# Optimization experiments

Measured on AMD Instinct MI355X. Metric: run time of the kernel, lower is better.

Reference implementation:

```python
import jax, jax.numpy as jnp
import numpy as np

B, S, E, H, F = 4, 1024, 1024, 16, 4096
D = E // H
DEPTH = 3
EPS_LN = 1e-5
EPS_ENT = 1e-6


def setup_inputs() -> dict:
    key = jax.random.key(0)
    ks = jax.random.split(key, 32)
    def w(k, shp, s=0.02):
        return (jax.random.normal(k, shp) * s).astype(jnp.float32)
    z = lambda *shp: jnp.zeros(shp, jnp.float32)
    inp = {
        'x': jax.random.normal(ks[0], (B, S, E), jnp.float32),
        # self-referential attention
        'sr_w': w(ks[1], (E, E)), 'sr_b': z(E),
        'q_w': w(ks[2], (E, E)), 'q_b': z(E),
        'k_w': w(ks[3], (E, E)), 'k_b': z(E),
        'v_w': w(ks[4], (E, E)), 'v_b': z(E),
        'o_w': w(ks[5], (E, E)), 'o_b': z(E),
        'ref_gate': jnp.float32(0.5),
        # quantum-classical interface
        'c_w': w(ks[6], (E, E)), 'c_b': z(E),
        'qp_w': w(ks[7], (E, E)), 'qp_b': z(E),
        'ig_w': w(ks[8], (2 * E, E)), 'ig_b': z(E),
        'temperature': jnp.float32(1.0),
        # entropy regulator
        'kp_w': w(ks[9], (E, E)), 'kp_b': z(E),
        'ee_w': w(ks[10], (E, 1)), 'ee_b': z(1),
        'eta': jnp.float32(0.1),
        # ffn
        'f1_w': w(ks[11], (E, F)), 'f1_b': z(F),
        'f2_w': w(ks[12], (F, E)), 'f2_b': z(E),
        # layernorms
        'ln1_g': jnp.ones(E, jnp.float32), 'ln1_b': z(E),
        'ln2_g': jnp.ones(E, jnp.float32), 'ln2_b': z(E),
        'ln3_g': jnp.ones(E, jnp.float32), 'ln3_b': z(E),
        # observer
        'obs_w': w(ks[13], (E, E)), 'obs_b': z(E),
        'obs_gate': jnp.float32(0.2),
    }
    return inp


def _lin(x, W, b):
    return x @ W + b


def _ln(x, g, b):
    m = jnp.mean(x, -1, keepdims=True)
    v = jnp.var(x, -1, keepdims=True)
    return (x - m) * jax.lax.rsqrt(v + EPS_LN) * g + b


def _layer(x, p):
    ks = jax.lax.stop_gradient(x)  # knowledge_state = x.detach()
    scale = 1.0 / (D ** 0.5)
    for _ in range(DEPTH):  # fixed small recursion depth
        # --- self-referential attention on norm1(x) ---
        xn = _ln(x, p['ln1_g'], p['ln1_b'])
        xr = xn + p['ref_gate'] * _lin(xn, p['sr_w'], p['sr_b'])
        b, s, _ = xn.shape
        q = _lin(xr, p['q_w'], p['q_b']).reshape(b, s, H, D)
        k = _lin(xr, p['k_w'], p['k_b']).reshape(b, s, H, D)
        v = _lin(xn, p['v_w'], p['v_b']).reshape(b, s, H, D)
        scores = jnp.einsum('bqhd,bkhd->bhqk', q, k) * scale  # [B,H,S,S]
        aw = jax.nn.softmax(scores, axis=-1)
        ao = jnp.einsum('bhqk,bkhd->bqhd', aw, v).reshape(b, s, E)
        quantum = _lin(ao, p['o_w'], p['o_b'])
        # --- FFN on norm2(x) (dropout = identity, eval mode) ---
        xn2 = _ln(x, p['ln2_g'], p['ln2_b'])
        h = jax.nn.gelu(_lin(xn2, p['f1_w'], p['f1_b']), approximate=False)
        classical = _lin(h, p['f2_w'], p['f2_b'])
        # --- quantum-classical interface ---
        c_proj = _lin(classical, p['c_w'], p['c_b'])
        q_proj = _lin(quantum, p['qp_w'], p['qp_b'])
        gate = jax.nn.sigmoid(_lin(jnp.concatenate([c_proj, q_proj], -1), p['ig_w'], p['ig_b']))
        sim = jnp.einsum('bqe,bke->bqk', c_proj, q_proj) / (E ** 0.5)  # [B,S,S]
        attw = jax.nn.softmax(sim / p['temperature'], axis=-1)
        transfer = jnp.einsum('bqk,bke->bqe', attw, quantum)
        iface = classical + gate * transfer
        # --- entropy regulator ---
        logp = jax.nn.log_softmax(iface, axis=-1)
        entropy = -jnp.sum(jnp.exp(logp) * logp, -1, keepdims=True)
        neg_entropy = _lin(ks, p['kp_w'], p['kp_b'])
        bal = jax.nn.sigmoid(_lin(iface, p['ee_w'], p['ee_b']))
        regulated = iface + p['eta'] * bal * (neg_entropy / (entropy + EPS_ENT))
        # --- residual + observer feedback + knowledge update ---
        x = x + regulated
        x = x + p['obs_gate'] * _lin(x, p['obs_w'], p['obs_b'])
        ks = ks + 0.1 * (x - ks)
    x = _ln(x, p['ln3_g'], p['ln3_b'])
    return x, ks


def reference(x, sr_w, sr_b, q_w, q_b, k_w, k_b, v_w, v_b, o_w, o_b, ref_gate,
              c_w, c_b, qp_w, qp_b, ig_w, ig_b, temperature,
              kp_w, kp_b, ee_w, ee_b, eta,
              f1_w, f1_b, f2_w, f2_b,
              ln1_g, ln1_b, ln2_g, ln2_b, ln3_g, ln3_b,
              obs_w, obs_b, obs_gate):
    p = dict(sr_w=sr_w, sr_b=sr_b, q_w=q_w, q_b=q_b, k_w=k_w, k_b=k_b,
             v_w=v_w, v_b=v_b, o_w=o_w, o_b=o_b, ref_gate=ref_gate,
             c_w=c_w, c_b=c_b, qp_w=qp_w, qp_b=qp_b, ig_w=ig_w, ig_b=ig_b,
             temperature=temperature, kp_w=kp_w, kp_b=kp_b, ee_w=ee_w, ee_b=ee_b,
             eta=eta, f1_w=f1_w, f1_b=f1_b, f2_w=f2_w, f2_b=f2_b,
             ln1_g=ln1_g, ln1_b=ln1_b, ln2_g=ln2_g, ln2_b=ln2_b,
             ln3_g=ln3_g, ln3_b=ln3_b, obs_w=obs_w, obs_b=obs_b, obs_gate=obs_gate)
    return _layer(x, p)
```

## Files before the change

kernel.cpp:

```cpp
#include <hip/hip_runtime.h>
#include <hip/hip_bf16.h>
#include <cmath>


typedef unsigned short u16;
typedef short v8s __attribute__((ext_vector_type(8)));
typedef float v4f __attribute__((ext_vector_type(4)));
typedef unsigned short u16x4 __attribute__((ext_vector_type(4)));

#define DEV __device__ __forceinline__

DEV float b2f(u16 u) { return __uint_as_float(((unsigned int)u) << 16); }
DEV u16 f2b(float f) {
    unsigned int x = __float_as_uint(f);
    return (u16)((x + 0x7fffu + ((x >> 16) & 1u)) >> 16);
}
DEV bool badf(float f) { return ((__float_as_uint(f) >> 23) & 0xFF) == 0xFF; }

DEV void async16(const void* g, void* l) {
    __builtin_amdgcn_global_load_lds((const __attribute__((address_space(1))) void*)g,
                                     (__attribute__((address_space(3))) void*)l, 16, 0, 0);
}

struct InArr { const void* p[37]; int n[37]; };
struct BJobs { int si[20]; int off[20]; int n[20]; };
struct GJ2 { const u16* jA; const u16* jB; const u16* jbias; u16* jout; };

#define CLS_CAP 131072

__global__ void reset_k(int* diag, int* cnt) {
    if (threadIdx.x == 0) *diag = 0x7FFFFFFF;
    if (threadIdx.x < 80) cnt[threadIdx.x] = 0;
}

__global__ void classify_k(InArr A, int* cnt) {
    int i = blockIdx.y;
    int n = A.n[i];
    if (n <= 1) return;
    const u16* q = (const u16*)A.p[i];
    long pairs = n >> 1;
    int wild = 0, pz = 0;
    if (pairs > (long)CLS_CAP) {
        long chunk = CLS_CAP / gridDim.x;
        long p0 = (long)blockIdx.x * (pairs / gridDim.x);
        for (long j = p0 + threadIdx.x; j < p0 + chunk; j += blockDim.x) {
            u16 w0 = q[2 * j], w1 = q[2 * j + 1];
            wild += ((w0 & 0x7FFF) >= 0x5000) + ((w1 & 0x7FFF) >= 0x5000);
            pz += (w0 == 0 && w1 >= 0x3000 && w1 <= 0x4100) ? 1 : 0;
        }
    } else {
        long stride = (long)gridDim.x * blockDim.x;
        for (long j = (long)blockIdx.x * blockDim.x + threadIdx.x; j < pairs; j += stride) {
            u16 w0 = q[2 * j], w1 = q[2 * j + 1];
            wild += ((w0 & 0x7FFF) >= 0x5000) + ((w1 & 0x7FFF) >= 0x5000);
            pz += (w0 == 0 && w1 >= 0x3000 && w1 <= 0x4100) ? 1 : 0;
        }
    }
#pragma unroll
    for (int off = 1; off < 64; off <<= 1) {
        wild += __shfl_xor(wild, off);
        pz += __shfl_xor(pz, off);
    }
    if ((threadIdx.x & 63) == 0) {
        atomicAdd(&cnt[2 * i], wild);
        atomicAdd(&cnt[2 * i + 1], pz);
    }
}

__global__ void finalize_k(InArr A, const int* cnt, int* flags) {
    int i = threadIdx.x;
    if (i < 37) {
        int n = A.n[i];
        int f = 0;
        if (n > 1) {
            long pairs = (long)n >> 1;
            long wthr, pthr;
            if (pairs > (long)CLS_CAP) { wthr = (2L * CLS_CAP) >> 6; pthr = (long)CLS_CAP >> 2; }
            else { wthr = (long)n >> 6; pthr = (long)n >> 3; }
            f = (cnt[2 * i] > wthr) || (cnt[2 * i + 1] > pthr);
        }
        flags[i] = f;
    }
}

DEV float dec_scalar(const u16* p) {
    float bf = b2f(p[0]);
    if (bf > 0.0009765625f && bf < 8.0f) return bf;
    unsigned int w = (((unsigned int)p[1]) << 16) | (unsigned int)p[0];
    return __uint_as_float(w);
}

__global__ void decode_scalars_k(const u16* rg, const u16* tp, const u16* et,
                                 const u16* og, float* out)
{
    if (threadIdx.x == 0 && blockIdx.x == 0) {
        out[0] = dec_scalar(rg);
        out[1] = dec_scalar(tp);
        out[2] = dec_scalar(et);
        out[3] = dec_scalar(og);
    }
}

__global__ void cvt1d_k(InArr A, BJobs J, const int* flags, u16* BIA) {
    int j = blockIdx.y;
    int n = J.n[j];
    int si = J.si[j];
    const void* src = A.p[si];
    u16* dst = BIA + (long)J.off[j] * 1024;
    int f = flags[si];
    int stride = gridDim.x * blockDim.x;
    for (int i = blockIdx.x * blockDim.x + threadIdx.x; i < n; i += stride) {
        dst[i] = f ? f2b(((const float*)src)[i]) : ((const u16*)src)[i];
    }
}

__global__ void chk_scal_k(const float* scal, int* diag) {
    if (threadIdx.x == 0) {
        for (int i = 0; i < 4; i++) {
            float v = scal[i];
            if (!(v > 0.f && v < 8.f)) atomicMin(diag, 3);
        }
    }
}

__global__ void fin32_k(float* out, long n4, const int* diag) {
    long stride = (long)gridDim.x * blockDim.x;
    long i0 = (long)blockIdx.x * blockDim.x + threadIdx.x;
    v4f* o4 = (v4f*)out;
    for (long i = i0; i < n4; i += stride) {
        v4f v = o4[i];
        bool b = false;
#pragma unroll
        for (int j = 0; j < 4; j++) b |= badf(v[j]);
        if (b) {
#pragma unroll
            for (int j = 0; j < 4; j++) if (badf(v[j])) v[j] = 0.f;
            o4[i] = v;
        }
    }
    if (i0 == 0) {
        int d = *diag;
        if (d != 0x7FFFFFFF) out[0] = 200.f + 4.f * (float)(d < 70 ? d : 70);
    }
}

__global__ void small_k(float* out, int code) {
    if (threadIdx.x == 0 && blockIdx.x == 0) out[0] = 900.f + 4.f * code;
}

__global__ __launch_bounds__(256) void f2c_k(const float* __restrict__ a, const float* __restrict__ b,
                                             const u16* __restrict__ bias, u16* __restrict__ out,
                                             int stage, int* __restrict__ diag)
{
    long i0 = ((long)blockIdx.x * 256 + threadIdx.x) * 4;
    v4f va = *(const v4f*)(a + i0);
    v4f vb = *(const v4f*)(b + i0);
    int colb = (int)(i0 & 1023);
    bool bad = false;
    u16x4 o;
#pragma unroll
    for (int j = 0; j < 4; j++) {
        float r = va[j] + vb[j] + b2f(bias[colb + j]);
        bad |= badf(r);
        o[j] = f2b(r);
    }
    *(u16x4*)(out + i0) = o;
    if (__ballot(bad) && (threadIdx.x & 63) == 0) atomicMin(diag, stage);
}

template <int EPI>
__global__ __launch_bounds__(512) void gemm_bt(
    const u16* __restrict__ A, int lda, long sA,
    const u16* __restrict__ A2, int ksplit,
    const u16* __restrict__ Bt, int ldb, long sB,
    const u16* __restrict__ bias,
    u16* __restrict__ obf, float* __restrict__ of32, int ldc, long sC,
    int K,
    const float* __restrict__ scp,
    const u16* __restrict__ aux,
    float* __restrict__ xaux, float* __restrict__ ksf, u16* __restrict__ ksb,
    float* __restrict__ kso,
    GJ2 J2,
    int stage, int* __restrict__ diag)
{
    __shared__ __align__(16) u16 As[128 * 32];
    __shared__ __align__(16) u16 Bs[128 * 32];
    const int tid = threadIdx.x;
    const int w = tid >> 6, l = tid & 63;
    const int lr = l & 15, lq = l >> 4;

    const int gx = gridDim.x, gy = gridDim.y;
    const int nwg = gx * gy * (int)gridDim.z;
    int flat = blockIdx.x + gx * (blockIdx.y + gy * blockIdx.z);
    int qq = nwg >> 3, rr = nwg & 7;
    int xcd = flat & 7, loc = flat >> 3;
    int nf = (xcd < rr ? xcd * (qq + 1) : rr * (qq + 1) + (xcd - rr) * qq) + loc;
    const int bx = nf % gx;
    int tmp = nf / gx;
    const int by = tmp % gy;
    int z = tmp / gy;

    const u16* Aj = A; const u16* Bj = Bt; const u16* biasj = bias; u16* obfj = obf;
    if (J2.jA) {
        if (z == 1) { Aj = J2.jA; Bj = J2.jB; biasj = J2.jbias; obfj = J2.jout; }
        z = 0;
    }

    const int m0 = by * 128, n0 = bx * 128;
    const u16* Az = Aj + (long)z * sA;
    const u16* Bz = Bj + (long)z * sB;
    const int wm = (w >> 2) * 64, wn = (w & 3) * 32;

    v4f zero4 = {0.f, 0.f, 0.f, 0.f};
    v4f acc[4][2];
#pragma unroll
    for (int i = 0; i < 4; i++)
#pragma unroll
        for (int j = 0; j < 2; j++) acc[i][j] = zero4;

    const int srow = tid >> 2, scc = (tid & 3) * 8;
    for (int k0 = 0; k0 < K; k0 += 32) {
        __syncthreads();
        const u16* Ab = (k0 < ksplit) ? (Az + k0) : (A2 + (k0 - ksplit));
        async16(Ab + (long)(m0 + srow) * lda + scc, (char*)As + w * 1024);
        async16(Bz + (long)(n0 + srow) * ldb + k0 + scc, (char*)Bs + w * 1024);
        __syncthreads();
        v8s av[4], bv[2];
#pragma unroll
        for (int mi = 0; mi < 4; mi++) av[mi] = *(const v8s*)(As + (wm + mi * 16 + lr) * 32 + lq * 8);
#pragma unroll
        for (int ni = 0; ni < 2; ni++) bv[ni] = *(const v8s*)(Bs + (wn + ni * 16 + lr) * 32 + lq * 8);
#pragma unroll
        for (int mi = 0; mi < 4; mi++)
#pragma unroll
            for (int ni = 0; ni < 2; ni++)
                acc[mi][ni] = __builtin_amdgcn_mfma_f32_16x16x32_bf16(av[mi], bv[ni], acc[mi][ni], 0, 0, 0);
    }

    float gsv = 0.f;
    if (EPI == 4 || EPI == 5 || EPI == 6) gsv = scp[0];
    if (EPI == 4) gsv = fmaxf(gsv, 1e-8f);
    bool bad = false;
#pragma unroll
    for (int mi = 0; mi < 4; mi++) {
        int row = m0 + wm + mi * 16 + lq * 4;
#pragma unroll
        for (int ni = 0; ni < 2; ni++) {
            int col = n0 + wn + ni * 16 + lr;
            float bb = biasj ? b2f(biasj[col]) : 0.f;
#pragma unroll
            for (int r = 0; r < 4; r++) {
                float v = acc[mi][ni][r] + bb;
                if (EPI == 6 || EPI == 7) {
                    long rbase = (long)(row + r) * 1024;
                    float res;
                    if (col < 1024) {
                        res = (EPI == 6) ? (b2f(aux[rbase + col]) + gsv * v) : v;
                        bad |= badf(res);
                        obfj[rbase + col] = f2b(res);
                    } else {
                        res = v;
                        bad |= badf(res);
                        J2.jout[rbase + col - 1024] = f2b(res);
                    }
                } else {
                    long idx = (long)z * sC + (long)(row + r) * ldc + col;
                    float res = v;
                    if (EPI == 2) res = 0.5f * v * (1.f + erff(v * 0.70710678118654752f));
                    else if (EPI == 3) res = 1.f / (1.f + expf(-v));
                    else if (EPI == 4) res = v * (0.03125f / gsv);
                    else if (EPI == 5) {
                        float xv = xaux[idx];
                        float nx = xv + gsv * v;
                        xaux[idx] = nx;
                        float kv = ksf[idx];
                        float kn = kv + 0.1f * (nx - kv);
                        ksf[idx] = kn;
                        ksb[idx] = f2b(kn);
                        if (kso) kso[idx] = kn;
                        bad |= badf(kn);
                        res = nx;
                    }
                    bad |= badf(res);
                    if (obfj) obfj[idx] = f2b(res);
                    if (of32) of32[idx] = res;
                }
            }
        }
    }
    if (__ballot(bad) && l == 0) atomicMin(diag, stage);
}

__global__ __launch_bounds__(256) void flash_k(
    const u16* __restrict__ q, const u16* __restrict__ k, const u16* __restrict__ v,
    u16* __restrict__ ao, int stage, int* __restrict__ diag)
{
    __shared__ __align__(16) u16 Ks[64 * 64];
    __shared__ __align__(16) u16 Vt[64 * 64];
    __shared__ __align__(16) u16 Pw[4 * 16 * 64];
    const int tid = threadIdx.x, w = tid >> 6, l = tid & 63;
    const int lr = l & 15, lq = l >> 4;
    const int bh = blockIdx.y, b = bh >> 4, h = bh & 15;
    const long rowbase = (long)b * 1024;
    const int h64 = h * 64;
    const int q0 = blockIdx.x * 64;

    const u16* Qp = q + (rowbase + q0 + w * 16 + lr) * 1024 + h64;
    v8s aq0 = *(const v8s*)(Qp + lq * 8);
    v8s aq1 = *(const v8s*)(Qp + 32 + lq * 8);

    v4f zero4 = {0.f, 0.f, 0.f, 0.f};
    v4f oacc[4];
    float m_r[4], l_r[4];
#pragma unroll
    for (int i = 0; i < 4; i++) { oacc[i] = zero4; m_r[i] = -INFINITY; l_r[i] = 0.f; }

    const int ss = lr & 7;
    const int colk = (lq ^ ss) << 3;
    u16* Pp = Pw + w * (16 * 64);

    for (int kt = 0; kt < 16; kt++) {
        __syncthreads();
        const long kbase = rowbase + kt * 64;
#pragma unroll
        for (int p = 0; p < 2; p++) {
            int c = p * 256 + tid;
            int row = c >> 3;
            int sl = (c & 7) ^ (row & 7);
            async16(k + (kbase + row) * 1024 + h64 + sl * 8, (char*)Ks + p * 4096 + w * 1024);
            int cc = (c & 7) * 8;
            v8s vv = *(const v8s*)(v + (kbase + row) * 1024 + h64 + cc);
#pragma unroll
            for (int j = 0; j < 8; j++) {
                int d = cc + j;
                int g = (d & 7) ^ ((d >> 3) & 7);
                Vt[((d << 6) + row) ^ (g << 3)] = (u16)vv[j];
            }
        }
        __syncthreads();

        v4f s[4];
#pragma unroll
        for (int nt = 0; nt < 4; nt++) {
            const u16* Kr = Ks + ((nt * 16 + lr) << 6);
            v8s b0 = *(const v8s*)(Kr + colk);
            v8s b1 = *(const v8s*)(Kr + (colk ^ 32));
            v4f t = zero4;
            t = __builtin_amdgcn_mfma_f32_16x16x32_bf16(aq0, b0, t, 0, 0, 0);
            t = __builtin_amdgcn_mfma_f32_16x16x32_bf16(aq1, b1, t, 0, 0, 0);
            s[nt] = t;
        }
#pragma unroll
        for (int r = 0; r < 4; r++) {
#pragma unroll
            for (int nt = 0; nt < 4; nt++) s[nt][r] *= 0.125f;
            float mx = fmaxf(fmaxf(s[0][r], s[1][r]), fmaxf(s[2][r], s[3][r]));
#pragma unroll
            for (int off = 1; off < 16; off <<= 1) mx = fmaxf(mx, __shfl_xor(mx, off));
            float mn = fmaxf(m_r[r], mx);
            float al = __expf(m_r[r] - mn);
            float rs = 0.f;
            int qrow = lq * 4 + r;
            int pbase = qrow << 6;
            int pswz = (qrow & 7) << 3;
#pragma unroll
            for (int nt = 0; nt < 4; nt++) {
                float pv = __expf(s[nt][r] - mn);
                rs += pv;
                Pp[pbase + ((nt * 16 + lr) ^ pswz)] = f2b(pv);
            }
#pragma unroll
            for (int off = 1; off < 16; off <<= 1) rs += __shfl_xor(rs, off);
            l_r[r] = l_r[r] * al + rs;
            m_r[r] = mn;
#pragma unroll
            for (int nt = 0; nt < 4; nt++) oacc[nt][r] *= al;
        }
        const u16* Pr = Pp + (lr << 6);
        v8s pa0 = *(const v8s*)(Pr + colk);
        v8s pa1 = *(const v8s*)(Pr + (colk ^ 32));
#pragma unroll
        for (int nt = 0; nt < 4; nt++) {
            const u16* Vr = Vt + ((nt * 16 + lr) << 6);
            int gv = (ss ^ (2 * nt + (lr >> 3))) << 3;
            int colv = (lq << 3) ^ gv;
            v8s vb0 = *(const v8s*)(Vr + colv);
            v8s vb1 = *(const v8s*)(Vr + (colv ^ 32));
            oacc[nt] = __builtin_amdgcn_mfma_f32_16x16x32_bf16(pa0, vb0, oacc[nt], 0, 0, 0);
            oacc[nt] = __builtin_amdgcn_mfma_f32_16x16x32_bf16(pa1, vb1, oacc[nt], 0, 0, 0);
        }
    }
    bool bad = false;
#pragma unroll
    for (int r = 0; r < 4; r++) {
        float inv = 1.f / l_r[r];
#pragma unroll
        for (int nt = 0; nt < 4; nt++) {
            float val = oacc[nt][r] * inv;
            bad |= badf(val);
            ao[(rowbase + q0 + w * 16 + lq * 4 + r) * 1024 + h64 + nt * 16 + lr] = f2b(val);
        }
    }
    if (__ballot(bad) && l == 0) atomicMin(diag, stage);
}

template <int F32OUT>
__global__ __launch_bounds__(256) void ln_k(const float* __restrict__ x,
                                            const u16* __restrict__ g, const u16* __restrict__ bt,
                                            u16* __restrict__ outb, float* __restrict__ outf,
                                            int stage, int* __restrict__ diag)
{
    __shared__ float red[8];
    int row = blockIdx.x, t = threadIdx.x, w = t >> 6;
    const float* xr = x + (long)row * 1024;
    float v[4], s = 0.f, sq = 0.f;
#pragma unroll
    for (int i = 0; i < 4; i++) { v[i] = xr[i * 256 + t]; s += v[i]; sq += v[i] * v[i]; }
#pragma unroll
    for (int off = 1; off < 64; off <<= 1) { s += __shfl_xor(s, off); sq += __shfl_xor(sq, off); }
    if ((t & 63) == 0) { red[w] = s; red[4 + w] = sq; }
    __syncthreads();
    float S = red[0] + red[1] + red[2] + red[3];
    float SQ = red[4] + red[5] + red[6] + red[7];
    float mean = S * (1.f / 1024.f);
    float var = fmaxf(SQ * (1.f / 1024.f) - mean * mean, 0.f);
    float rs = rsqrtf(var + 1e-5f);
    bool bad = false;
#pragma unroll
    for (int i = 0; i < 4; i++) {
        int e = i * 256 + t;
        float r = (v[i] - mean) * rs * b2f(g[e]) + b2f(bt[e]);
        bad |= badf(r);
        if (F32OUT) outf[(long)row * 1024 + e] = r;
        else outb[(long)row * 1024 + e] = f2b(r);
    }
    if (__ballot(bad) && (t & 63) == 0) atomicMin(diag, stage);
}

__global__ __launch_bounds__(256) void rowfuse_k(
    const u16* __restrict__ cls, const u16* __restrict__ gate, const float* __restrict__ tr,
    const u16* __restrict__ ne, const u16* __restrict__ eew, const u16* __restrict__ eeb,
    const float* __restrict__ eta_p, float* __restrict__ xbuf, u16* __restrict__ x1b,
    int stage, int* __restrict__ diag)
{
    __shared__ float red[16];
    int row = blockIdx.x, t = threadIdx.x, w = t >> 6;
    long base = (long)row * 1024;
    float ifc[4];
#pragma unroll
    for (int i = 0; i < 4; i++) {
        int e = i * 256 + t;
        ifc[i] = b2f(cls[base + e]) + b2f(gate[base + e]) * tr[base + e];
    }
    float mx = fmaxf(fmaxf(ifc[0], ifc[1]), fmaxf(ifc[2], ifc[3]));
#pragma unroll
    for (int off = 1; off < 64; off <<= 1) mx = fmaxf(mx, __shfl_xor(mx, off));
    if ((t & 63) == 0) red[w] = mx;
    __syncthreads();
    float MX = fmaxf(fmaxf(red[0], red[1]), fmaxf(red[2], red[3]));
    float s1 = 0.f, s2 = 0.f, dot = 0.f;
#pragma unroll
    for (int i = 0; i < 4; i++) {
        int e = i * 256 + t;
        float ex = expf(ifc[i] - MX);
        s1 += ex; s2 += ex * ifc[i]; dot += ifc[i] * b2f(eew[e]);
    }
#pragma unroll
    for (int off = 1; off < 64; off <<= 1) {
        s1 += __shfl_xor(s1, off); s2 += __shfl_xor(s2, off); dot += __shfl_xor(dot, off);
    }
    if ((t & 63) == 0) { red[4 + w] = s1; red[8 + w] = s2; red[12 + w] = dot; }
    __syncthreads();
    float S1 = red[4] + red[5] + red[6] + red[7];
    float S2 = red[8] + red[9] + red[10] + red[11];
    float DT = red[12] + red[13] + red[14] + red[15];
    float logZ = MX + logf(S1);
    float ent = logZ - S2 / S1;
    float bal = 1.f / (1.f + expf(-(DT + b2f(eeb[0]))));
    float fac = eta_p[0] * bal / (ent + 1e-6f);
    bool bad = false;
#pragma unroll
    for (int i = 0; i < 4; i++) {
        int e = i * 256 + t;
        float rg = ifc[i] + fac * b2f(ne[base + e]);
        float x1 = xbuf[base + e] + rg;
        bad |= badf(x1);
        xbuf[base + e] = x1;
        x1b[base + e] = f2b(x1);
    }
    if (__ballot(bad) && (t & 63) == 0) atomicMin(diag, stage);
}

__global__ __launch_bounds__(256) void softmax_k(const float* __restrict__ sim, u16* __restrict__ out,
                                                 int stage, int* __restrict__ diag)
{
    __shared__ float red[8];
    int row = blockIdx.x, t = threadIdx.x, w = t >> 6;
    long base = (long)row * 1024;
    float v[4];
#pragma unroll
    for (int i = 0; i < 4; i++) v[i] = sim[base + i * 256 + t];
    float mx = fmaxf(fmaxf(v[0], v[1]), fmaxf(v[2], v[3]));
#pragma unroll
    for (int off = 1; off < 64; off <<= 1) mx = fmaxf(mx, __shfl_xor(mx, off));
    if ((t & 63) == 0) red[w] = mx;
    __syncthreads();
    float MX = fmaxf(fmaxf(red[0], red[1]), fmaxf(red[2], red[3]));
    float s = 0.f;
#pragma unroll
    for (int i = 0; i < 4; i++) { v[i] = expf(v[i] - MX); s += v[i]; }
#pragma unroll
    for (int off = 1; off < 64; off <<= 1) s += __shfl_xor(s, off);
    if ((t & 63) == 0) red[4 + w] = s;
    __syncthreads();
    float inv = 1.f / (red[4] + red[5] + red[6] + red[7]);
    bool bad = false;
#pragma unroll
    for (int i = 0; i < 4; i++) {
        float o = v[i] * inv;
        bad |= badf(o);
        out[base + i * 256 + t] = f2b(o);
    }
    if (__ballot(bad) && (t & 63) == 0) atomicMin(diag, stage);
}

__global__ void transpose_ft_k(const void* __restrict__ in, u16* __restrict__ out,
                               int R, int C, const int* __restrict__ flags, int idx,
                               int* __restrict__ diag)
{
    __shared__ u16 tile[32][33];
    int f = flags[idx];
    int x = blockIdx.x * 32 + threadIdx.x;
    int y0 = blockIdx.y * 32;
#pragma unroll
    for (int j = 0; j < 4; j++) {
        long src = (long)(y0 + threadIdx.y + j * 8) * C + x;
        tile[threadIdx.y + j * 8][threadIdx.x] =
            f ? f2b(((const float*)in)[src]) : ((const u16*)in)[src];
    }
    __syncthreads();
    int ox = y0 + threadIdx.x;
    int oy0 = blockIdx.x * 32;
    bool bad = false;
#pragma unroll
    for (int j = 0; j < 4; j++) {
        u16 u = tile[threadIdx.x][threadIdx.y + j * 8];
        bad |= ((u & 0x7FFF) >= 0x7F80);
        out[(long)(oy0 + threadIdx.y + j * 8) * R + ox] = u;
    }
    if (__ballot(bad) && ((threadIdx.y * 32 + threadIdx.x) & 63) == 0) atomicMin(diag, 2);
}

__global__ void transpose_k(const u16* __restrict__ in, u16* __restrict__ out,
                            int R, int C, long sIn, long sOut)
{
    __shared__ u16 tile[32][33];
    int z = blockIdx.z;
    in += (long)z * sIn; out += (long)z * sOut;
    int x = blockIdx.x * 32 + threadIdx.x;
    int y0 = blockIdx.y * 32;
#pragma unroll
    for (int j = 0; j < 4; j++)
        tile[threadIdx.y + j * 8][threadIdx.x] = in[(long)(y0 + threadIdx.y + j * 8) * C + x];
    __syncthreads();
    int ox = y0 + threadIdx.x;
    int oy0 = blockIdx.x * 32;
#pragma unroll
    for (int j = 0; j < 4; j++)
        out[(long)(oy0 + threadIdx.y + j * 8) * R + ox] = tile[threadIdx.x][threadIdx.y + j * 8];
}

__global__ __launch_bounds__(256) void init_k(const void* __restrict__ xin, const int* __restrict__ flags,
                                              float* __restrict__ xbuf,
                                              float* __restrict__ ksf, u16* __restrict__ ksb,
                                              int* __restrict__ diag)
{
    int t = threadIdx.x;
    int f = flags[0];
    long base = (long)blockIdx.x * 1024;
    bool bad = false;
#pragma unroll
    for (int i = 0; i < 4; i++) {
        long idx = base + i * 256 + t;
        float xv = f ? ((const float*)xin)[idx] : b2f(((const u16*)xin)[idx]);
        bad |= badf(xv);
        xbuf[idx] = xv; ksf[idx] = xv; ksb[idx] = f2b(xv);
    }
    if (__ballot(bad) && (t & 63) == 0) atomicMin(diag, 1);
}

extern "C" void kernel_launch(void* const* d_in, const int* in_sizes, int n_in,
                              void* d_out, int out_size, void* d_ws, size_t ws_size,
                              hipStream_t stream)
{
    const size_t MB = 1u << 20;
    float* outf = (float*)d_out;
    if (ws_size < 192 * MB) {
        int code = (int)(ws_size >> 25); if (code > 9) code = 9;
        small_k<<<1, 64, 0, stream>>>(outf, code);
        return;
    }
    const u16* s_refg = (const u16*)d_in[11];
    const u16* s_temp = (const u16*)d_in[18];
    const u16* s_eta  = (const u16*)d_in[23];
    const u16* s_obsg = (const u16*)d_in[36];

    InArr IA;
    for (int i = 0; i < 37; i++) { IA.p[i] = d_in[i]; IA.n[i] = (i < n_in) ? in_sizes[i] : 0; }

    char* ws = (char*)d_ws;
    u16* srT  = (u16*)(ws + 0 * MB);
    u16* vT   = (u16*)(ws + 2 * MB);
    u16* qT   = (u16*)(ws + 4 * MB);
    u16* kT   = (u16*)(ws + 6 * MB);
    u16* oT   = (u16*)(ws + 8 * MB);
    u16* cT   = (u16*)(ws + 10 * MB);
    u16* qpT  = (u16*)(ws + 12 * MB);
    u16* kpT  = (u16*)(ws + 14 * MB);
    u16* obsT = (u16*)(ws + 16 * MB);
    u16* igT  = (u16*)(ws + 18 * MB);
    u16* f1T  = (u16*)(ws + 22 * MB);
    u16* f2T  = (u16*)(ws + 30 * MB);
    float* scal = (float*)(ws + 38 * MB);
    int* diag  = (int*)(ws + 38 * MB + 64);
    int* flags = (int*)(ws + 38 * MB + 128);
    int* cnt   = (int*)(ws + 38 * MB + 512);
    u16* BIA   = (u16*)(ws + 38 * MB + 8192);
    u16* c_bsr = BIA + 0*1024,  *c_bv = BIA + 1*1024;
    u16* c_bq  = BIA + 2*1024,  *c_bk = BIA + 3*1024;
    u16* c_bo  = BIA + 4*1024,  *c_bc = BIA + 5*1024;
    u16* c_bqp = BIA + 6*1024,  *c_big = BIA + 7*1024, *c_bkp = BIA + 8*1024;
    u16* c_bobs= BIA + 9*1024,  *c_bf2 = BIA + 10*1024;
    u16* c_g1  = BIA + 11*1024, *c_be1 = BIA + 12*1024;
    u16* c_g2  = BIA + 13*1024, *c_be2 = BIA + 14*1024;
    u16* c_g3  = BIA + 15*1024, *c_be3 = BIA + 16*1024;
    u16* c_eew = BIA + 17*1024, *c_eeb = BIA + 18*1024;
    u16* c_bf1 = BIA + 19*1024;
    float* xbuf = (float*)(ws + 40 * MB);
    float* ksf  = (float*)(ws + 56 * MB);
    u16* ksb    = (u16*)(ws + 72 * MB);
    u16* xn     = (u16*)(ws + 80 * MB);
    u16* xn2    = (u16*)(ws + 88 * MB);
    u16* xr     = (u16*)(ws + 96 * MB);
    u16* qb     = (u16*)(ws + 104 * MB);
    u16* kb     = (u16*)(ws + 112 * MB);
    u16* vb     = (u16*)(ws + 120 * MB);
    u16* aob    = (u16*)(ws + 128 * MB);
    u16* quant  = (u16*)(ws + 136 * MB);
    u16* hb     = (u16*)(ws + 144 * MB);
    float* simf = (float*)(ws + 144 * MB);
    float* trf  = (float*)(ws + 160 * MB);
    u16* clsb   = (u16*)(ws + 176 * MB);
    u16* neb    = (u16*)(ws + 184 * MB);
    float* f2pa = (float*)(ws + 104 * MB);
    float* f2pb = (float*)(ws + 120 * MB);
    u16* quantT = xn;
    u16* cpb = qb;  u16* qpb = kb;  u16* gateb = vb;  u16* attw = aob;  u16* x1b = xr;

    const long BS1 = 1024L * 1024L;
    const int KBIG = 1 << 30;
    dim3 tb(32, 8), blk(256), gblk(512);
    GJ2 J0 = {nullptr, nullptr, nullptr, nullptr};

    auto G = [&](int epi, int gx, int gy, int gz,
                 const u16* A, int lda, long sA, const u16* A2, int ksp,
                 const u16* Bt, int ldb, long sB, const u16* bias,
                 u16* obf, float* of32, int ldc, long sC, int K,
                 const float* scp, const u16* aux, float* xa, float* kf, u16* kb2, float* kso,
                 GJ2 J2, int stg) {
        dim3 grid(gx, gy, gz);
        switch (epi) {
            case 0: gemm_bt<0><<<grid, gblk, 0, stream>>>(A, lda, sA, A2, ksp, Bt, ldb, sB, bias, obf, of32, ldc, sC, K, scp, aux, xa, kf, kb2, kso, J2, stg, diag); break;
            case 2: gemm_bt<2><<<grid, gblk, 0, stream>>>(A, lda, sA, A2, ksp, Bt, ldb, sB, bias, obf, of32, ldc, sC, K, scp, aux, xa, kf, kb2, kso, J2, stg, diag); break;
            case 3: gemm_bt<3><<<grid, gblk, 0, stream>>>(A, lda, sA, A2, ksp, Bt, ldb, sB, bias, obf, of32, ldc, sC, K, scp, aux, xa, kf, kb2, kso, J2, stg, diag); break;
            case 4: gemm_bt<4><<<grid, gblk, 0, stream>>>(A, lda, sA, A2, ksp, Bt, ldb, sB, bias, obf, of32, ldc, sC, K, scp, aux, xa, kf, kb2, kso, J2, stg, diag); break;
            case 5: gemm_bt<5><<<grid, gblk, 0, stream>>>(A, lda, sA, A2, ksp, Bt, ldb, sB, bias, obf, of32, ldc, sC, K, scp, aux, xa, kf, kb2, kso, J2, stg, diag); break;
            case 6: gemm_bt<6><<<grid, gblk, 0, stream>>>(A, lda, sA, A2, ksp, Bt, ldb, sB, bias, obf, of32, ldc, sC, K, scp, aux, xa, kf, kb2, kso, J2, stg, diag); break;
            case 7: gemm_bt<7><<<grid, gblk, 0, stream>>>(A, lda, sA, A2, ksp, Bt, ldb, sB, bias, obf, of32, ldc, sC, K, scp, aux, xa, kf, kb2, kso, J2, stg, diag); break;
            case 8: gemm_bt<8><<<grid, gblk, 0, stream>>>(A, lda, sA, A2, ksp, Bt, ldb, sB, bias, obf, of32, ldc, sC, K, scp, aux, xa, kf, kb2, kso, J2, stg, diag); break;
        }
    };

    reset_k<<<1, 256, 0, stream>>>(diag, cnt);
    classify_k<<<dim3(64, 37), blk, 0, stream>>>(IA, cnt);
    finalize_k<<<1, 64, 0, stream>>>(IA, cnt, flags);
    decode_scalars_k<<<1, 64, 0, stream>>>(s_refg, s_temp, s_eta, s_obsg, scal);
    BJobs BJ = {
        {2, 8, 4, 6, 10, 13, 15, 17, 20, 35, 27, 28, 29, 30, 31, 32, 33, 21, 22, 25},
        {0, 1, 2, 3, 4, 5, 6, 7, 8, 9, 10, 11, 12, 13, 14, 15, 16, 17, 18, 19},
        {1024,1024,1024,1024,1024,1024,1024,1024,1024,1024,1024,1024,1024,1024,1024,1024,1024,1024,1,4096}
    };
    cvt1d_k<<<dim3(4, 20), blk, 0, stream>>>(IA, BJ, flags, BIA);
    struct WT { int idx; u16* dst; long n; int R, C, gx, gy; };
    WT wts[12] = {
        {1, srT, 1048576, 1024, 1024, 32, 32},  {7, vT, 1048576, 1024, 1024, 32, 32},
        {3, qT, 1048576, 1024, 1024, 32, 32},   {5, kT, 1048576, 1024, 1024, 32, 32},
        {9, oT, 1048576, 1024, 1024, 32, 32},   {12, cT, 1048576, 1024, 1024, 32, 32},
        {14, qpT, 1048576, 1024, 1024, 32, 32}, {19, kpT, 1048576, 1024, 1024, 32, 32},
        {34, obsT, 1048576, 1024, 1024, 32, 32},
        {16, igT, 2097152, 2048, 1024, 32, 64},
        {24, f1T, 4194304, 1024, 4096, 128, 32},
        {26, f2T, 4194304, 4096, 1024, 32, 128},
    };
    for (int i = 0; i < 12; i++) {
        transpose_ft_k<<<dim3(wts[i].gx, wts[i].gy, 1), tb, 0, stream>>>(
            d_in[wts[i].idx], wts[i].dst, wts[i].R, wts[i].C, flags, wts[i].idx, diag);
    }
    init_k<<<4096, blk, 0, stream>>>(d_in[0], flags, xbuf, ksf, ksb, diag);
    chk_scal_k<<<1, 64, 0, stream>>>(scal, diag);

    for (int it = 0; it < 3; it++) {
        int sb = 4 + it * 20;
        ln_k<0><<<4096, blk, 0, stream>>>(xbuf, c_g1, c_be1, xn, nullptr, sb + 0, diag);
        GJ2 Jsrv = {nullptr, nullptr, nullptr, vb};
        G(6, 16, 32, 1, xn, 1024, 0, nullptr, KBIG, srT, 1024, 0, c_bsr, xr, nullptr, 1024, 0, 1024, scal + 0, xn, nullptr, nullptr, nullptr, nullptr, Jsrv, sb + 1);
        GJ2 Jqk = {nullptr, nullptr, nullptr, kb};
        G(7, 16, 32, 1, xr, 1024, 0, nullptr, KBIG, qT, 1024, 0, c_bq, qb, nullptr, 1024, 0, 1024, nullptr, nullptr, nullptr, nullptr, nullptr, nullptr, Jqk, sb + 2);
        flash_k<<<dim3(16, 64), blk, 0, stream>>>(qb, kb, vb, aob, sb + 5, diag);
        GJ2 Jokp = {ksb, kpT, c_bkp, neb};
        G(0, 8, 32, 2, aob, 1024, 0, nullptr, KBIG, oT, 1024, 0, c_bo, quant, nullptr, 1024, 0, 1024, nullptr, nullptr, nullptr, nullptr, nullptr, nullptr, Jokp, sb + 6);
        transpose_k<<<dim3(32, 32, 4), tb, 0, stream>>>(quant, quantT, 1024, 1024, BS1, BS1);
        ln_k<0><<<4096, blk, 0, stream>>>(xbuf, c_g2, c_be2, xn2, nullptr, sb + 7, diag);
        G(2, 32, 32, 1, xn2, 1024, 0, nullptr, KBIG, f1T, 1024, 0, c_bf1, hb, nullptr, 4096, 0, 1024, nullptr, nullptr, nullptr, nullptr, nullptr, nullptr, J0, sb + 8);
        G(8, 8, 32, 2, hb, 4096, 2048, nullptr, KBIG, f2T, 4096, 2048, nullptr, nullptr, f2pa, 1024, 4194304, 2048, nullptr, nullptr, nullptr, nullptr, nullptr, nullptr, J0, sb + 9);
        f2c_k<<<4096, blk, 0, stream>>>(f2pa, f2pb, c_bf2, clsb, sb + 9, diag);
        GJ2 Jcqp = {quant, qpT, c_bqp, qpb};
        G(0, 8, 32, 2, clsb, 1024, 0, nullptr, KBIG, cT, 1024, 0, c_bc, cpb, nullptr, 1024, 0, 1024, nullptr, nullptr, nullptr, nullptr, nullptr, nullptr, Jcqp, sb + 10);
        G(3, 8, 32, 1, cpb, 1024, 0, qpb, 1024, igT, 2048, 0, c_big, gateb, nullptr, 1024, 0, 2048, nullptr, nullptr, nullptr, nullptr, nullptr, nullptr, J0, sb + 12);
        G(4, 8, 8, 4, cpb, 1024, BS1, nullptr, KBIG, qpb, 1024, BS1, nullptr, nullptr, simf, 1024, BS1, 1024, scal + 1, nullptr, nullptr, nullptr, nullptr, nullptr, J0, sb + 14);
        softmax_k<<<4096, blk, 0, stream>>>(simf, attw, sb + 15, diag);
        G(0, 8, 8, 4, attw, 1024, BS1, nullptr, KBIG, quantT, 1024, BS1, nullptr, nullptr, trf, 1024, BS1, 1024, nullptr, nullptr, nullptr, nullptr, nullptr, nullptr, J0, sb + 16);
        rowfuse_k<<<4096, blk, 0, stream>>>(clsb, gateb, trf, neb, c_eew, c_eeb, scal + 2, xbuf, x1b, sb + 17, diag);
        float* kso = (it == 2) ? (outf + 4194304) : nullptr;
        G(5, 8, 32, 1, x1b, 1024, 0, nullptr, KBIG, obsT, 1024, 0, c_bobs, nullptr, nullptr, 1024, 0, 1024, scal + 3, nullptr, xbuf, ksf, ksb, kso, J0, sb + 18);
    }
    ln_k<1><<<4096, blk, 0, stream>>>(xbuf, c_g3, c_be3, nullptr, outf, 70, diag);
    fin32_k<<<1024, blk, 0, stream>>>(outf, 2097152, diag);
}
```

Baseline: 1.772 ms.

## Double GEMM K-tile to 64 with XOR-swizzled LDS and remap flash blocks per XCD

The bf16 GEMM now stages a 64-wide K slice per iteration instead of 32. Each thread issues two async global-to-LDS copies into an XOR-swizzled layout. Fragment reads undo the swizzle, which avoids LDS bank conflicts and halves the number of barrier pairs per unit of K. The flash attention kernel remaps its flat block index so blocks landing on the same XCD share the same (batch, head), which improves L2 reuse of K/V. The cost is doubled LDS use in the GEMM, which may lower occupancy, and the flash remap hardcodes the 16x64 grid shape.

```diff
diff --git a/kernel.cpp b/kernel.cpp
--- a/kernel.cpp
+++ b/kernel.cpp
@@ -183,8 +183,8 @@
     GJ2 J2,
     int stage, int* __restrict__ diag)
 {
-    __shared__ __align__(16) u16 As[128 * 32];
-    __shared__ __align__(16) u16 Bs[128 * 32];
+    __shared__ __align__(16) u16 As[128 * 64];
+    __shared__ __align__(16) u16 Bs[128 * 64];
     const int tid = threadIdx.x;
     const int w = tid >> 6, l = tid & 63;
     const int lr = l & 15, lq = l >> 4;
@@ -218,23 +218,44 @@
 #pragma unroll
         for (int j = 0; j < 2; j++) acc[i][j] = zero4;
 
-    const int srow = tid >> 2, scc = (tid & 3) * 8;
-    for (int k0 = 0; k0 < K; k0 += 32) {
+    const int swz = lr & 7;
+    const int c0s = (lq ^ swz) << 3;
+    const int c1s = ((lq + 4) ^ swz) << 3;
+    for (int k0 = 0; k0 < K; k0 += 64) {
         __syncthreads();
         const u16* Ab = (k0 < ksplit) ? (Az + k0) : (A2 + (k0 - ksplit));
-        async16(Ab + (long)(m0 + srow) * lda + scc, (char*)As + w * 1024);
-        async16(Bz + (long)(n0 + srow) * ldb + k0 + scc, (char*)Bs + w * 1024);
+#pragma unroll
+        for (int p = 0; p < 2; p++) {
+            int c = p * 512 + tid;
+            int row = c >> 3;
+            int sc = ((c & 7) ^ (row & 7)) * 8;
+            async16(Ab + (long)(m0 + row) * lda + sc, (char*)As + p * 8192 + w * 1024);
+            async16(Bz + (long)(n0 + row) * ldb + k0 + sc, (char*)Bs + p * 8192 + w * 1024);
+        }
         __syncthreads();
-        v8s av[4], bv[2];
-#pragma unroll
-        for (int mi = 0; mi < 4; mi++) av[mi] = *(const v8s*)(As + (wm + mi * 16 + lr) * 32 + lq * 8);
-#pragma unroll
-        for (int ni = 0; ni < 2; ni++) bv[ni] = *(const v8s*)(Bs + (wn + ni * 16 + lr) * 32 + lq * 8);
+        v8s av0[4], av1[4], bv0[2], bv1[2];
+#pragma unroll
+        for (int mi = 0; mi < 4; mi++) {
+            const u16* Ar = As + ((wm + mi * 16 + lr) << 6);
+            av0[mi] = *(const v8s*)(Ar + c0s);
+            av1[mi] = *(const v8s*)(Ar + c1s);
+        }
+#pragma unroll
+        for (int ni = 0; ni < 2; ni++) {
+            const u16* Br = Bs + ((wn + ni * 16 + lr) << 6);
+            bv0[ni] = *(const v8s*)(Br + c0s);
+            bv1[ni] = *(const v8s*)(Br + c1s);
+        }
 #pragma unroll
         for (int mi = 0; mi < 4; mi++)
 #pragma unroll
             for (int ni = 0; ni < 2; ni++)
-                acc[mi][ni] = __builtin_amdgcn_mfma_f32_16x16x32_bf16(av[mi], bv[ni], acc[mi][ni], 0, 0, 0);
+                acc[mi][ni] = __builtin_amdgcn_mfma_f32_16x16x32_bf16(av0[mi], bv0[ni], acc[mi][ni], 0, 0, 0);
+#pragma unroll
+        for (int mi = 0; mi < 4; mi++)
+#pragma unroll
+            for (int ni = 0; ni < 2; ni++)
+                acc[mi][ni] = __builtin_amdgcn_mfma_f32_16x16x32_bf16(av1[mi], bv1[ni], acc[mi][ni], 0, 0, 0);
     }
 
     float gsv = 0.f;
@@ -300,10 +321,13 @@
     __shared__ __align__(16) u16 Pw[4 * 16 * 64];
     const int tid = threadIdx.x, w = tid >> 6, l = tid & 63;
     const int lr = l & 15, lq = l >> 4;
-    const int bh = blockIdx.y, b = bh >> 4, h = bh & 15;
+    const int flat = blockIdx.x + (blockIdx.y << 4);
+    const int xcd = flat & 7, loc = flat >> 3;
+    const int bh = xcd * 8 + (loc >> 4);
+    const int q0 = (loc & 15) * 64;
+    const int b = bh >> 4, h = bh & 15;
     const long rowbase = (long)b * 1024;
     const int h64 = h * 64;
-    const int q0 = blockIdx.x * 64;
 
     const u16* Qp = q + (rowbase + q0 + w * 16 + lr) * 1024 + h64;
     v8s aq0 = *(const v8s*)(Qp + lq * 8);
```

Result: faster. 1.656 ms (-6.5%).
